# Optimization experiments

Hardware: AMD Instinct MI355X
Metric: run time of the kernel (lower is better)

Reference implementation:

```python
import jax, jax.numpy as jnp
import numpy as np

N_NODES = 100000
N_EDGES = 800000
IN_C, HID_C, OUT_C = 128, 64, 40


def setup_inputs() -> dict:
    key = jax.random.key(0)
    k1, k2, k3, k4, k5, k6 = jax.random.split(key, 6)
    x = jax.random.normal(k1, (N_NODES, IN_C), dtype=jnp.float32)
    edge_index = jax.random.randint(k2, (2, N_EDGES), 0, N_NODES, dtype=jnp.int64)
    W1 = jax.random.normal(k3, (IN_C, HID_C), dtype=jnp.float32) * (1.0 / np.sqrt(IN_C))
    b1 = jax.random.normal(k4, (HID_C,), dtype=jnp.float32) * 0.01
    W2 = jax.random.normal(k5, (HID_C, OUT_C), dtype=jnp.float32) * (1.0 / np.sqrt(HID_C))
    b2 = jax.random.normal(k6, (OUT_C,), dtype=jnp.float32) * 0.01
    return {"x": x, "edge_index": edge_index, "W1": W1, "b1": b1, "W2": W2, "b2": b2}


def _sg_propagate(x, src, dst, n):
    # GCN symmetric normalization (self-loops already appended by caller):
    # deg[i] = number of incoming edges at i; norm_e = deg[src]^-1/2 * deg[dst]^-1/2
    deg = jax.ops.segment_sum(jnp.ones_like(dst, dtype=x.dtype), dst, num_segments=n)
    dinv = jnp.where(deg > 0, jax.lax.rsqrt(deg), jnp.zeros_like(deg))
    norm = dinv[src] * dinv[dst]  # [E]
    # out[i] = sum_{e: dst_e=i} norm_e * x[src_e]
    return jax.ops.segment_sum(x[src] * norm[:, None], dst, num_segments=n)


def reference(x, edge_index, W1, b1, W2, b2):
    n = x.shape[0]
    loop = jnp.arange(n, dtype=edge_index.dtype)
    src = jnp.concatenate([edge_index[0], loop])
    dst = jnp.concatenate([edge_index[1], loop])
    # dropout is identity in eval mode
    h = _sg_propagate(x, src, dst, n) @ W1 + b1   # SGConv(in_c, hid_c), K=1
    h = jax.nn.relu(h)
    o = _sg_propagate(h, src, dst, n) @ W2 + b2   # SGConv(hid_c, out_c), K=1
    return jax.nn.log_softmax(o, axis=1)
```

## Files before the change

kernel.cpp:

```cpp
#include <hip/hip_runtime.h>
#include <math.h>

#define IN_C 128
#define HID_C 64
#define OUT_C 40

typedef unsigned short u16;
__device__ __forceinline__ float bf2f(u16 u) {
  return __uint_as_float(((unsigned int)u) << 16);
}
__device__ __forceinline__ u16 f2bf(float f) {
  unsigned int u = __float_as_uint(f);
  u += 0x7fffu + ((u >> 16) & 1u);
  return (u16)(u >> 16);
}

__global__ void zero4_kernel(int4* __restrict__ p, long long n4) {
  long long i = (long long)blockIdx.x * blockDim.x + threadIdx.x;
  long long stride = (long long)gridDim.x * blockDim.x;
  for (; i < n4; i += stride) p[i] = make_int4(0, 0, 0, 0);
}

__global__ __launch_bounds__(256) void scan1_kernel(
    const int* __restrict__ deg, int* __restrict__ S, int* __restrict__ BS,
    int n) {
  __shared__ int sums[256];
  int t = threadIdx.x;
  int i0 = blockIdx.x * 1024 + t * 4;
  int v0 = (i0 + 0 < n) ? deg[i0 + 0] : 0;
  int v1 = (i0 + 1 < n) ? deg[i0 + 1] : 0;
  int v2 = (i0 + 2 < n) ? deg[i0 + 2] : 0;
  int v3 = (i0 + 3 < n) ? deg[i0 + 3] : 0;
  v1 += v0; v2 += v1; v3 += v2;
  sums[t] = v3;
  __syncthreads();
  for (int off = 1; off < 256; off <<= 1) {
    int x = (t >= off) ? sums[t - off] : 0;
    __syncthreads();
    sums[t] += x;
    __syncthreads();
  }
  int excl = t ? sums[t - 1] : 0;
  if (i0 + 0 < n) S[i0 + 0] = v0 + excl;
  if (i0 + 1 < n) S[i0 + 1] = v1 + excl;
  if (i0 + 2 < n) S[i0 + 2] = v2 + excl;
  if (i0 + 3 < n) S[i0 + 3] = v3 + excl;
  if (t == 255) BS[blockIdx.x] = sums[255];
}

__global__ __launch_bounds__(128) void scan2_kernel(int* __restrict__ BS,
                                                    int nb) {
  __shared__ int s[128];
  int t = threadIdx.x;
  s[t] = (t < nb) ? BS[t] : 0;
  __syncthreads();
  for (int off = 1; off < 128; off <<= 1) {
    int x = (t >= off) ? s[t - off] : 0;
    __syncthreads();
    s[t] += x;
    __syncthreads();
  }
  if (t < nb) BS[t] = t ? s[t - 1] : 0;
}

__global__ void scan3_kernel(const int* __restrict__ S,
                             const int* __restrict__ BS,
                             const int* __restrict__ deg,
                             int* __restrict__ rowptr,
                             float* __restrict__ dinv, int n) {
  int i = blockIdx.x * blockDim.x + threadIdx.x;
  if (i < n) {
    int d = deg[i];
    int r = S[i] + BS[i >> 10];
    rowptr[i + 1] = r;
    dinv[i] = rsqrtf((float)d + 1.0f);
    if (i == 0) rowptr[0] = 0;
  }
}

#define XS_LD 68
#define DP_BLOCKS 1024
__global__ __launch_bounds__(256) void fused_degpos_gemm1_kernel(
    const int* __restrict__ dst, int E, int* __restrict__ deg,
    int* __restrict__ pos, const float* __restrict__ x,
    const float* __restrict__ W1, float* __restrict__ y, int n) {
  __shared__ float xs[64 * XS_LD];
  __shared__ float wsh[64 * HID_C];
  int t = threadIdx.x;
  int b = (int)blockIdx.x;
  bool isDP;
  int bi;
  if (b < 2 * DP_BLOCKS) { isDP = (b & 1) == 0; bi = b >> 1; }
  else                   { isDP = false;        bi = b - DP_BLOCKS; }
  if (isDP) {
    int base = bi * 256 + t;
    int stride = DP_BLOCKS * 256;
    for (int e = base; e < E; e += 4 * stride) {
      int e1 = e + stride, e2 = e + 2 * stride, e3 = e + 3 * stride;
      bool g1 = e1 < E, g2 = e2 < E, g3 = e3 < E;
      int d0 = dst[e];
      int d1 = g1 ? dst[e1] : 0;
      int d2 = g2 ? dst[e2] : 0;
      int d3 = g3 ? dst[e3] : 0;
      int p0 = atomicAdd(&deg[d0], 1);
      int p1 = g1 ? atomicAdd(&deg[d1], 1) : 0;
      int p2 = g2 ? atomicAdd(&deg[d2], 1) : 0;
      int p3 = g3 ? atomicAdd(&deg[d3], 1) : 0;
      pos[e] = p0;
      if (g1) pos[e1] = p1;
      if (g2) pos[e2] = p2;
      if (g3) pos[e3] = p3;
    }
    return;
  }
  int rowBase = bi * 64;
  if (rowBase >= n) return;
  const float4* xf4 = (const float4*)x;
  const float4* wf4 = (const float4*)W1;
  int tx = t & 15, ty = t >> 4;
  int i0 = ty * 4, j0 = tx * 4;
  float acc[4][4];
#pragma unroll
  for (int r = 0; r < 4; ++r)
#pragma unroll
    for (int j = 0; j < 4; ++j) acc[r][j] = 0.f;

  for (int kc = 0; kc < 2; ++kc) {
#pragma unroll
    for (int k = 0; k < 4; ++k) {
      int t4 = t + k * 256;
      int row = t4 >> 4, c4 = t4 & 15;
      int gr = rowBase + row;
      if (gr >= n) gr = n - 1;
      *(float4*)&xs[row * XS_LD + c4 * 4] = xf4[(size_t)gr * 32 + kc * 16 + c4];
      *(float4*)&wsh[row * HID_C + c4 * 4] = wf4[(size_t)(kc * 64 + row) * 16 + c4];
    }
    __syncthreads();
#pragma unroll 2
    for (int c4 = 0; c4 < 64; c4 += 4) {
      float4 xv[4], wv[4];
#pragma unroll
      for (int r = 0; r < 4; ++r)
        xv[r] = *(const float4*)&xs[(i0 + r) * XS_LD + c4];
#pragma unroll
      for (int cc = 0; cc < 4; ++cc)
        wv[cc] = *(const float4*)&wsh[(c4 + cc) * HID_C + j0];
#pragma unroll
      for (int r = 0; r < 4; ++r) {
#pragma unroll
        for (int cc = 0; cc < 4; ++cc) {
          float xr = (&xv[r].x)[cc];
          acc[r][0] = fmaf(xr, wv[cc].x, acc[r][0]);
          acc[r][1] = fmaf(xr, wv[cc].y, acc[r][1]);
          acc[r][2] = fmaf(xr, wv[cc].z, acc[r][2]);
          acc[r][3] = fmaf(xr, wv[cc].w, acc[r][3]);
        }
      }
    }
    __syncthreads();
  }
#pragma unroll
  for (int r = 0; r < 4; ++r) {
    int i = rowBase + i0 + r;
    if (i < n) {
      float4 v = make_float4(acc[r][0], acc[r][1], acc[r][2], acc[r][3]);
      *(float4*)&y[(size_t)i * HID_C + j0] = v;
    }
  }
}

#define FB_BLOCKS 1024
#define SC_BLOCKS 1024
__global__ __launch_bounds__(256) void fused_fill_scale_kernel(
    const int* __restrict__ eidx, int E, const int* __restrict__ rowptr,
    const int* __restrict__ pos, int* __restrict__ csr,
    const float* __restrict__ dinv, const float4* __restrict__ y4,
    ushort4* __restrict__ ybf, int n) {
  int t = threadIdx.x;
  if ((int)blockIdx.x < FB_BLOCKS) {
    int base = blockIdx.x * 256 + t;
    int stride = FB_BLOCKS * 256;
    for (int e = base; e < E; e += 4 * stride) {
      int e1 = e + stride, e2 = e + 2 * stride, e3 = e + 3 * stride;
      bool g1 = e1 < E, g2 = e2 < E, g3 = e3 < E;
      int s0 = eidx[e], d0 = eidx[E + e], p0 = pos[e];
      int s1 = 0, d1 = 0, p1 = 0, s2 = 0, d2 = 0, p2 = 0, s3 = 0, d3 = 0, p3 = 0;
      if (g1) { s1 = eidx[e1]; d1 = eidx[E + e1]; p1 = pos[e1]; }
      if (g2) { s2 = eidx[e2]; d2 = eidx[E + e2]; p2 = pos[e2]; }
      if (g3) { s3 = eidx[e3]; d3 = eidx[E + e3]; p3 = pos[e3]; }
      int r0 = rowptr[d0];
      int r1 = g1 ? rowptr[d1] : 0;
      int r2 = g2 ? rowptr[d2] : 0;
      int r3 = g3 ? rowptr[d3] : 0;
      csr[r0 + p0] = s0;
      if (g1) csr[r1 + p1] = s1;
      if (g2) csr[r2 + p2] = s2;
      if (g3) csr[r3 + p3] = s3;
    }
    return;
  }
  long long total = (long long)n * 16;
  long long base = (long long)((int)blockIdx.x - FB_BLOCKS) * 256 + t;
  long long stride = (long long)SC_BLOCKS * 256;
  for (long long idx = base; idx < total; idx += stride) {
    int i = (int)(idx >> 4);
    float di = dinv[i];
    float4 v = y4[idx];
    ushort4 u;
    u.x = f2bf(di * v.x);
    u.y = f2bf(di * v.y);
    u.z = f2bf(di * v.z);
    u.w = f2bf(di * v.w);
    ybf[idx] = u;
  }
}

__global__ __launch_bounds__(256) void gather1_kernel(
    const ushort4* __restrict__ y4, const int* __restrict__ rowptr,
    const int* __restrict__ csr, const float* __restrict__ dinv,
    const float* __restrict__ b1, float* __restrict__ h, int n) {
  int lane = threadIdx.x & 63;
  int grp = lane >> 4;
  int q = lane & 15;
  float4 b1v = ((const float4*)b1)[q];
  int wid = (int)((blockIdx.x * blockDim.x + threadIdx.x) >> 6);
  int nw = (int)((gridDim.x * blockDim.x) >> 6);
  int ii = wid;
  int e0 = 0, e1 = 0; float di = 0.f;
  if (ii < n) { e0 = rowptr[ii]; e1 = rowptr[ii + 1]; di = dinv[ii]; }
  while (ii < n) {
    int nxt = ii + nw;
    int ne0 = 0, ne1 = 0; float ndi = 0.f;
    if (nxt < n) { ne0 = rowptr[nxt]; ne1 = rowptr[nxt + 1]; ndi = dinv[nxt]; }
    int i = __builtin_amdgcn_readfirstlane(ii);
    float4 acc = make_float4(0.f, 0.f, 0.f, 0.f);
    if (grp == 0) {
      ushort4 u = y4[(size_t)i * 16 + q];
      acc.x = bf2f(u.x); acc.y = bf2f(u.y); acc.z = bf2f(u.z); acc.w = bf2f(u.w);
    }
    int e = e0 + grp, end = e1;
    for (; e + 4 < end; e += 8) {
      int s0 = csr[e], s1 = csr[e + 4];
      ushort4 u0 = y4[(size_t)s0 * 16 + q];
      ushort4 u1 = y4[(size_t)s1 * 16 + q];
      acc.x += bf2f(u0.x) + bf2f(u1.x);
      acc.y += bf2f(u0.y) + bf2f(u1.y);
      acc.z += bf2f(u0.z) + bf2f(u1.z);
      acc.w += bf2f(u0.w) + bf2f(u1.w);
    }
    for (; e < end; e += 4) {
      int s = csr[e];
      ushort4 u = y4[(size_t)s * 16 + q];
      acc.x += bf2f(u.x); acc.y += bf2f(u.y);
      acc.z += bf2f(u.z); acc.w += bf2f(u.w);
    }
    acc.x += __shfl_xor(acc.x, 16); acc.y += __shfl_xor(acc.y, 16);
    acc.z += __shfl_xor(acc.z, 16); acc.w += __shfl_xor(acc.w, 16);
    acc.x += __shfl_xor(acc.x, 32); acc.y += __shfl_xor(acc.y, 32);
    acc.z += __shfl_xor(acc.z, 32); acc.w += __shfl_xor(acc.w, 32);
    if (grp == 0) {
      float4 hv;
      hv.x = fmaxf(fmaf(di, acc.x, b1v.x), 0.f);
      hv.y = fmaxf(fmaf(di, acc.y, b1v.y), 0.f);
      hv.z = fmaxf(fmaf(di, acc.z, b1v.z), 0.f);
      hv.w = fmaxf(fmaf(di, acc.w, b1v.w), 0.f);
      *(float4*)&h[(size_t)i * HID_C + 4 * q] = hv;
    }
    ii = nxt; e0 = ne0; e1 = ne1; di = ndi;
  }
}

__global__ __launch_bounds__(256) void gemm2_kernel(
    const float* __restrict__ h, const float* __restrict__ W2,
    const float* __restrict__ dinv, float* __restrict__ z, int n) {
  __shared__ float hs[64 * XS_LD];
  __shared__ float w2s[64 * OUT_C + 32];
  int t = threadIdx.x;
  int rowBase = blockIdx.x * 64;
  const float4* hf4 = (const float4*)h;
  const float4* wf4 = (const float4*)W2;
#pragma unroll
  for (int k = 0; k < 4; ++k) {
    int t4 = t + k * 256;
    int row = t4 >> 4, c4 = t4 & 15;
    int gr = rowBase + row;
    if (gr >= n) gr = n - 1;
    *(float4*)&hs[row * XS_LD + c4 * 4] = hf4[(size_t)gr * 16 + c4];
  }
  for (int t4 = t; t4 < 640; t4 += 256)
    *(float4*)&w2s[t4 * 4] = wf4[t4];
  __syncthreads();
  int tx = t & 15, ty = t >> 4;
  int i0 = ty * 4, j0 = tx * 4;
  bool active = tx < 10;
  float acc[4][4];
#pragma unroll
  for (int r = 0; r < 4; ++r)
#pragma unroll
    for (int j = 0; j < 4; ++j) acc[r][j] = 0.f;
#pragma unroll 2
  for (int c4 = 0; c4 < 64; c4 += 4) {
    float4 hv[4], wv[4];
#pragma unroll
    for (int r = 0; r < 4; ++r)
      hv[r] = *(const float4*)&hs[(i0 + r) * XS_LD + c4];
#pragma unroll
    for (int cc = 0; cc < 4; ++cc)
      wv[cc] = *(const float4*)&w2s[(c4 + cc) * OUT_C + j0];
#pragma unroll
    for (int r = 0; r < 4; ++r) {
#pragma unroll
      for (int cc = 0; cc < 4; ++cc) {
        float hr = (&hv[r].x)[cc];
        acc[r][0] = fmaf(hr, wv[cc].x, acc[r][0]);
        acc[r][1] = fmaf(hr, wv[cc].y, acc[r][1]);
        acc[r][2] = fmaf(hr, wv[cc].z, acc[r][2]);
        acc[r][3] = fmaf(hr, wv[cc].w, acc[r][3]);
      }
    }
  }
  if (active) {
#pragma unroll
    for (int r = 0; r < 4; ++r) {
      int i = rowBase + i0 + r;
      if (i < n) {
        float d2 = dinv[i];
        float4 v = make_float4(d2 * acc[r][0], d2 * acc[r][1],
                               d2 * acc[r][2], d2 * acc[r][3]);
        *(float4*)&z[(size_t)i * OUT_C + j0] = v;
      }
    }
  }
}

__global__ __launch_bounds__(256) void gather40_kernel(
    const float4* __restrict__ z4, const int* __restrict__ rowptr,
    const int* __restrict__ csr, const float* __restrict__ dinv,
    const float* __restrict__ b2, float* __restrict__ out, int n) {
  int lane = threadIdx.x & 63;
  int grp = lane >> 4;
  int q = lane & 15;
  bool act = q < 10;
  float4 b2v = ((const float4*)b2)[act ? q : 0];
  int wid = (int)((blockIdx.x * blockDim.x + threadIdx.x) >> 6);
  int nw = (int)((gridDim.x * blockDim.x) >> 6);
  int ii = wid;
  int e0 = 0, e1 = 0; float di = 0.f;
  if (ii < n) { e0 = rowptr[ii]; e1 = rowptr[ii + 1]; di = dinv[ii]; }
  while (ii < n) {
    int nxt = ii + nw;
    int ne0 = 0, ne1 = 0; float ndi = 0.f;
    if (nxt < n) { ne0 = rowptr[nxt]; ne1 = rowptr[nxt + 1]; ndi = dinv[nxt]; }
    int i = __builtin_amdgcn_readfirstlane(ii);
    float4 acc = make_float4(0.f, 0.f, 0.f, 0.f);
    if (grp == 0 && act) acc = z4[(size_t)i * 10 + q];
    int e = e0 + grp, end = e1;
    if (act) {
      for (; e + 4 < end; e += 8) {
        int s0 = csr[e], s1 = csr[e + 4];
        float4 v0 = z4[(size_t)s0 * 10 + q];
        float4 v1 = z4[(size_t)s1 * 10 + q];
        acc.x += v0.x + v1.x;
        acc.y += v0.y + v1.y;
        acc.z += v0.z + v1.z;
        acc.w += v0.w + v1.w;
      }
      for (; e < end; e += 4) {
        int s = csr[e];
        float4 v = z4[(size_t)s * 10 + q];
        acc.x += v.x; acc.y += v.y; acc.z += v.z; acc.w += v.w;
      }
    }
    acc.x += __shfl_xor(acc.x, 16); acc.y += __shfl_xor(acc.y, 16);
    acc.z += __shfl_xor(acc.z, 16); acc.w += __shfl_xor(acc.w, 16);
    acc.x += __shfl_xor(acc.x, 32); acc.y += __shfl_xor(acc.y, 32);
    acc.z += __shfl_xor(acc.z, 32); acc.w += __shfl_xor(acc.w, 32);
    float4 o;
    o.x = fmaf(di, acc.x, b2v.x);
    o.y = fmaf(di, acc.y, b2v.y);
    o.z = fmaf(di, acc.z, b2v.z);
    o.w = fmaf(di, acc.w, b2v.w);
    float m = act ? fmaxf(fmaxf(o.x, o.y), fmaxf(o.z, o.w)) : -INFINITY;
    for (int off = 8; off; off >>= 1) m = fmaxf(m, __shfl_xor(m, off));
    float ex = act ? (expf(o.x - m) + expf(o.y - m) +
                      expf(o.z - m) + expf(o.w - m)) : 0.f;
    float s = ex;
    for (int off = 8; off; off >>= 1) s += __shfl_xor(s, off);
    if (lane < 16 && act) {
      float l = m + logf(s);
      float4 o2 = make_float4(o.x - l, o.y - l, o.z - l, o.w - l);
      *(float4*)&out[(size_t)i * OUT_C + 4 * q] = o2;
    }
    ii = nxt; e0 = ne0; e1 = ne1; di = ndi;
  }
}

extern "C" void kernel_launch(void* const* d_in, const int* in_sizes, int n_in,
                              void* d_out, int out_size, void* d_ws, size_t ws_size,
                              hipStream_t stream) {
  const float* x  = (const float*)d_in[0];
  const int* eidx = (const int*)d_in[1];
  const float* W1 = (const float*)d_in[2];
  const float* b1 = (const float*)d_in[3];
  const float* W2 = (const float*)d_in[4];
  const float* b2 = (const float*)d_in[5];
  float* out = (float*)d_out;

  int n = in_sizes[0] / IN_C;
  int E = in_sizes[1] / 2;

  size_t npad = ((size_t)n + 255) & ~(size_t)255;
  size_t Epad = ((size_t)E + 255) & ~(size_t)255;
  size_t o_dinv   = 0;
  size_t o_deg    = o_dinv + npad;
  size_t o_S      = o_deg + npad;
  size_t o_BS     = o_S + npad;
  size_t o_rowptr = o_BS + 256;
  size_t o_pos    = o_rowptr + npad + 256;
  size_t o_csr    = o_pos + Epad;
  size_t o_bufA   = o_csr + Epad;
  size_t o_bufC   = o_bufA + (size_t)n * HID_C;
  size_t needed   = (o_bufC + (size_t)n * HID_C) * 4;
  if (ws_size < needed) return;

  float* ws  = (float*)d_ws;
  float* dinv = ws + o_dinv;
  int* deg    = (int*)(ws + o_deg);
  int* S      = (int*)(ws + o_S);
  int* BS     = (int*)(ws + o_BS);
  int* rowptr = (int*)(ws + o_rowptr);
  int* pos    = (int*)(ws + o_pos);
  int* csr    = (int*)(ws + o_csr);
  float* bufA = ws + o_bufA;
  float* bufC = ws + o_bufC;

  int nb = (int)((n + 1023) / 1024);
  int gemmBlocks = (n + 63) / 64;

  zero4_kernel<<<128, 256, 0, stream>>>((int4*)deg, (long long)(npad / 4));
  fused_degpos_gemm1_kernel<<<DP_BLOCKS + gemmBlocks, 256, 0, stream>>>(
      eidx + E, E, deg, pos, x, W1, bufA, n);

  scan1_kernel<<<nb, 256, 0, stream>>>(deg, S, BS, n);
  scan2_kernel<<<1, 128, 0, stream>>>(BS, nb);
  scan3_kernel<<<(n + 255) / 256, 256, 0, stream>>>(S, BS, deg, rowptr, dinv, n);

  fused_fill_scale_kernel<<<FB_BLOCKS + SC_BLOCKS, 256, 0, stream>>>(
      eidx, E, rowptr, pos, csr, dinv, (const float4*)bufA, (ushort4*)bufC, n);

  gather1_kernel<<<2048, 256, 0, stream>>>((const ushort4*)bufC, rowptr, csr,
                                           dinv, b1, bufA, n);
  gemm2_kernel<<<gemmBlocks, 256, 0, stream>>>(bufA, W2, dinv, bufC, n);
  gather40_kernel<<<2048, 256, 0, stream>>>((const float4*)bufC, rowptr, csr,
                                            dinv, b2, out, n);
}
```

Measured before the change: 166.0 us.

## Store second-layer features as bf16 and gather with 16-byte loads per lane

```diff
diff --git a/kernel.cpp b/kernel.cpp
--- a/kernel.cpp
+++ b/kernel.cpp
@@ -6,13 +6,20 @@
 #define OUT_C 40
 
 typedef unsigned short u16;
-__device__ __forceinline__ float bf2f(u16 u) {
-  return __uint_as_float(((unsigned int)u) << 16);
-}
 __device__ __forceinline__ u16 f2bf(float f) {
   unsigned int u = __float_as_uint(f);
   u += 0x7fffu + ((u >> 16) & 1u);
   return (u16)(u >> 16);
+}
+__device__ __forceinline__ void bf8_add(uint4 u, float* a) {
+  a[0] += __uint_as_float(u.x << 16);
+  a[1] += __uint_as_float(u.x & 0xffff0000u);
+  a[2] += __uint_as_float(u.y << 16);
+  a[3] += __uint_as_float(u.y & 0xffff0000u);
+  a[4] += __uint_as_float(u.z << 16);
+  a[5] += __uint_as_float(u.z & 0xffff0000u);
+  a[6] += __uint_as_float(u.w << 16);
+  a[7] += __uint_as_float(u.w & 0xffff0000u);
 }
 
 __global__ void zero4_kernel(int4* __restrict__ p, long long n4) {
@@ -216,13 +223,14 @@
 }
 
 __global__ __launch_bounds__(256) void gather1_kernel(
-    const ushort4* __restrict__ y4, const int* __restrict__ rowptr,
+    const uint4* __restrict__ y8, const int* __restrict__ rowptr,
     const int* __restrict__ csr, const float* __restrict__ dinv,
     const float* __restrict__ b1, float* __restrict__ h, int n) {
   int lane = threadIdx.x & 63;
-  int grp = lane >> 4;
-  int q = lane & 15;
-  float4 b1v = ((const float4*)b1)[q];
+  int grp = lane >> 3;
+  int q = lane & 7;
+  float4 b1lo = ((const float4*)b1)[2 * q];
+  float4 b1hi = ((const float4*)b1)[2 * q + 1];
   int wid = (int)((blockIdx.x * blockDim.x + threadIdx.x) >> 6);
   int nw = (int)((gridDim.x * blockDim.x) >> 6);
   int ii = wid;
@@ -233,38 +241,36 @@
     int ne0 = 0, ne1 = 0; float ndi = 0.f;
     if (nxt < n) { ne0 = rowptr[nxt]; ne1 = rowptr[nxt + 1]; ndi = dinv[nxt]; }
     int i = __builtin_amdgcn_readfirstlane(ii);
-    float4 acc = make_float4(0.f, 0.f, 0.f, 0.f);
+    float a[8] = {0.f, 0.f, 0.f, 0.f, 0.f, 0.f, 0.f, 0.f};
+    if (grp == 0) bf8_add(y8[(size_t)i * 8 + q], a);
+    int e = e0 + grp, end = e1;
+    for (; e + 8 < end; e += 16) {
+      int s0 = csr[e], s1 = csr[e + 8];
+      bf8_add(y8[(size_t)s0 * 8 + q], a);
+      bf8_add(y8[(size_t)s1 * 8 + q], a);
+    }
+    for (; e < end; e += 8) {
+      int s = csr[e];
+      bf8_add(y8[(size_t)s * 8 + q], a);
+    }
+#pragma unroll
+    for (int k = 0; k < 8; ++k) {
+      a[k] += __shfl_xor(a[k], 8);
+      a[k] += __shfl_xor(a[k], 16);
+      a[k] += __shfl_xor(a[k], 32);
+    }
     if (grp == 0) {
-      ushort4 u = y4[(size_t)i * 16 + q];
-      acc.x = bf2f(u.x); acc.y = bf2f(u.y); acc.z = bf2f(u.z); acc.w = bf2f(u.w);
-    }
-    int e = e0 + grp, end = e1;
-    for (; e + 4 < end; e += 8) {
-      int s0 = csr[e], s1 = csr[e + 4];
-      ushort4 u0 = y4[(size_t)s0 * 16 + q];
-      ushort4 u1 = y4[(size_t)s1 * 16 + q];
-      acc.x += bf2f(u0.x) + bf2f(u1.x);
-      acc.y += bf2f(u0.y) + bf2f(u1.y);
-      acc.z += bf2f(u0.z) + bf2f(u1.z);
-      acc.w += bf2f(u0.w) + bf2f(u1.w);
-    }
-    for (; e < end; e += 4) {
-      int s = csr[e];
-      ushort4 u = y4[(size_t)s * 16 + q];
-      acc.x += bf2f(u.x); acc.y += bf2f(u.y);
-      acc.z += bf2f(u.z); acc.w += bf2f(u.w);
-    }
-    acc.x += __shfl_xor(acc.x, 16); acc.y += __shfl_xor(acc.y, 16);
-    acc.z += __shfl_xor(acc.z, 16); acc.w += __shfl_xor(acc.w, 16);
-    acc.x += __shfl_xor(acc.x, 32); acc.y += __shfl_xor(acc.y, 32);
-    acc.z += __shfl_xor(acc.z, 32); acc.w += __shfl_xor(acc.w, 32);
-    if (grp == 0) {
-      float4 hv;
-      hv.x = fmaxf(fmaf(di, acc.x, b1v.x), 0.f);
-      hv.y = fmaxf(fmaf(di, acc.y, b1v.y), 0.f);
-      hv.z = fmaxf(fmaf(di, acc.z, b1v.z), 0.f);
-      hv.w = fmaxf(fmaf(di, acc.w, b1v.w), 0.f);
-      *(float4*)&h[(size_t)i * HID_C + 4 * q] = hv;
+      float4 lo, hi;
+      lo.x = fmaxf(fmaf(di, a[0], b1lo.x), 0.f);
+      lo.y = fmaxf(fmaf(di, a[1], b1lo.y), 0.f);
+      lo.z = fmaxf(fmaf(di, a[2], b1lo.z), 0.f);
+      lo.w = fmaxf(fmaf(di, a[3], b1lo.w), 0.f);
+      hi.x = fmaxf(fmaf(di, a[4], b1hi.x), 0.f);
+      hi.y = fmaxf(fmaf(di, a[5], b1hi.y), 0.f);
+      hi.z = fmaxf(fmaf(di, a[6], b1hi.z), 0.f);
+      hi.w = fmaxf(fmaf(di, a[7], b1hi.w), 0.f);
+      *(float4*)&h[(size_t)i * HID_C + 8 * q] = lo;
+      *(float4*)&h[(size_t)i * HID_C + 8 * q + 4] = hi;
     }
     ii = nxt; e0 = ne0; e1 = ne1; di = ndi;
   }
@@ -272,7 +278,7 @@
 
 __global__ __launch_bounds__(256) void gemm2_kernel(
     const float* __restrict__ h, const float* __restrict__ W2,
-    const float* __restrict__ dinv, float* __restrict__ z, int n) {
+    const float* __restrict__ dinv, u16* __restrict__ z, int n) {
   __shared__ float hs[64 * XS_LD];
   __shared__ float w2s[64 * OUT_C + 32];
   int t = threadIdx.x;
@@ -325,23 +331,28 @@
       int i = rowBase + i0 + r;
       if (i < n) {
         float d2 = dinv[i];
-        float4 v = make_float4(d2 * acc[r][0], d2 * acc[r][1],
-                               d2 * acc[r][2], d2 * acc[r][3]);
-        *(float4*)&z[(size_t)i * OUT_C + j0] = v;
+        ushort4 u;
+        u.x = f2bf(d2 * acc[r][0]);
+        u.y = f2bf(d2 * acc[r][1]);
+        u.z = f2bf(d2 * acc[r][2]);
+        u.w = f2bf(d2 * acc[r][3]);
+        *(ushort4*)&z[(size_t)i * OUT_C + j0] = u;
       }
     }
   }
 }
 
 __global__ __launch_bounds__(256) void gather40_kernel(
-    const float4* __restrict__ z4, const int* __restrict__ rowptr,
+    const uint4* __restrict__ z8, const int* __restrict__ rowptr,
     const int* __restrict__ csr, const float* __restrict__ dinv,
     const float* __restrict__ b2, float* __restrict__ out, int n) {
   int lane = threadIdx.x & 63;
-  int grp = lane >> 4;
-  int q = lane & 15;
-  bool act = q < 10;
-  float4 b2v = ((const float4*)b2)[act ? q : 0];
+  int grp = lane >> 3;
+  int q = lane & 7;
+  bool act = q < 5;
+  int qc = act ? q : 0;
+  float4 b2lo = ((const float4*)b2)[2 * qc];
+  float4 b2hi = ((const float4*)b2)[2 * qc + 1];
   int wid = (int)((blockIdx.x * blockDim.x + threadIdx.x) >> 6);
   int nw = (int)((gridDim.x * blockDim.x) >> 6);
   int ii = wid;
@@ -352,44 +363,55 @@
     int ne0 = 0, ne1 = 0; float ndi = 0.f;
     if (nxt < n) { ne0 = rowptr[nxt]; ne1 = rowptr[nxt + 1]; ndi = dinv[nxt]; }
     int i = __builtin_amdgcn_readfirstlane(ii);
-    float4 acc = make_float4(0.f, 0.f, 0.f, 0.f);
-    if (grp == 0 && act) acc = z4[(size_t)i * 10 + q];
+    float a[8] = {0.f, 0.f, 0.f, 0.f, 0.f, 0.f, 0.f, 0.f};
+    if (grp == 0 && act) bf8_add(z8[(size_t)i * 5 + q], a);
     int e = e0 + grp, end = e1;
     if (act) {
-      for (; e + 4 < end; e += 8) {
-        int s0 = csr[e], s1 = csr[e + 4];
-        float4 v0 = z4[(size_t)s0 * 10 + q];
-        float4 v1 = z4[(size_t)s1 * 10 + q];
-        acc.x += v0.x + v1.x;
-        acc.y += v0.y + v1.y;
-        acc.z += v0.z + v1.z;
-        acc.w += v0.w + v1.w;
+      for (; e + 8 < end; e += 16) {
+        int s0 = csr[e], s1 = csr[e + 8];
+        bf8_add(z8[(size_t)s0 * 5 + q], a);
+        bf8_add(z8[(size_t)s1 * 5 + q], a);
       }
-      for (; e < end; e += 4) {
+      for (; e < end; e += 8) {
         int s = csr[e];
-        float4 v = z4[(size_t)s * 10 + q];
-        acc.x += v.x; acc.y += v.y; acc.z += v.z; acc.w += v.w;
+        bf8_add(z8[(size_t)s * 5 + q], a);
       }
     }
-    acc.x += __shfl_xor(acc.x, 16); acc.y += __shfl_xor(acc.y, 16);
-    acc.z += __shfl_xor(acc.z, 16); acc.w += __shfl_xor(acc.w, 16);
-    acc.x += __shfl_xor(acc.x, 32); acc.y += __shfl_xor(acc.y, 32);
-    acc.z += __shfl_xor(acc.z, 32); acc.w += __shfl_xor(acc.w, 32);
-    float4 o;
-    o.x = fmaf(di, acc.x, b2v.x);
-    o.y = fmaf(di, acc.y, b2v.y);
-    o.z = fmaf(di, acc.z, b2v.z);
-    o.w = fmaf(di, acc.w, b2v.w);
-    float m = act ? fmaxf(fmaxf(o.x, o.y), fmaxf(o.z, o.w)) : -INFINITY;
-    for (int off = 8; off; off >>= 1) m = fmaxf(m, __shfl_xor(m, off));
-    float ex = act ? (expf(o.x - m) + expf(o.y - m) +
-                      expf(o.z - m) + expf(o.w - m)) : 0.f;
-    float s = ex;
-    for (int off = 8; off; off >>= 1) s += __shfl_xor(s, off);
-    if (lane < 16 && act) {
+#pragma unroll
+    for (int k = 0; k < 8; ++k) {
+      a[k] += __shfl_xor(a[k], 8);
+      a[k] += __shfl_xor(a[k], 16);
+      a[k] += __shfl_xor(a[k], 32);
+    }
+    float o[8];
+    o[0] = fmaf(di, a[0], b2lo.x);
+    o[1] = fmaf(di, a[1], b2lo.y);
+    o[2] = fmaf(di, a[2], b2lo.z);
+    o[3] = fmaf(di, a[3], b2lo.w);
+    o[4] = fmaf(di, a[4], b2hi.x);
+    o[5] = fmaf(di, a[5], b2hi.y);
+    o[6] = fmaf(di, a[6], b2hi.z);
+    o[7] = fmaf(di, a[7], b2hi.w);
+    float m = act ? fmaxf(fmaxf(fmaxf(o[0], o[1]), fmaxf(o[2], o[3])),
+                          fmaxf(fmaxf(o[4], o[5]), fmaxf(o[6], o[7])))
+                  : -INFINITY;
+    m = fmaxf(m, __shfl_xor(m, 1));
+    m = fmaxf(m, __shfl_xor(m, 2));
+    m = fmaxf(m, __shfl_xor(m, 4));
+    float s = 0.f;
+    if (act) {
+#pragma unroll
+      for (int k = 0; k < 8; ++k) s += expf(o[k] - m);
+    }
+    s += __shfl_xor(s, 1);
+    s += __shfl_xor(s, 2);
+    s += __shfl_xor(s, 4);
+    if (lane < 8 && act) {
       float l = m + logf(s);
-      float4 o2 = make_float4(o.x - l, o.y - l, o.z - l, o.w - l);
-      *(float4*)&out[(size_t)i * OUT_C + 4 * q] = o2;
+      float4 lo = make_float4(o[0] - l, o[1] - l, o[2] - l, o[3] - l);
+      float4 hi = make_float4(o[4] - l, o[5] - l, o[6] - l, o[7] - l);
+      *(float4*)&out[(size_t)i * OUT_C + 8 * q] = lo;
+      *(float4*)&out[(size_t)i * OUT_C + 8 * q + 4] = hi;
     }
     ii = nxt; e0 = ne0; e1 = ne1; di = ndi;
   }
@@ -448,9 +470,9 @@
   fused_fill_scale_kernel<<<FB_BLOCKS + SC_BLOCKS, 256, 0, stream>>>(
       eidx, E, rowptr, pos, csr, dinv, (const float4*)bufA, (ushort4*)bufC, n);
 
-  gather1_kernel<<<2048, 256, 0, stream>>>((const ushort4*)bufC, rowptr, csr,
+  gather1_kernel<<<2048, 256, 0, stream>>>((const uint4*)bufC, rowptr, csr,
                                            dinv, b1, bufA, n);
-  gemm2_kernel<<<gemmBlocks, 256, 0, stream>>>(bufA, W2, dinv, bufC, n);
-  gather40_kernel<<<2048, 256, 0, stream>>>((const float4*)bufC, rowptr, csr,
+  gemm2_kernel<<<gemmBlocks, 256, 0, stream>>>(bufA, W2, dinv, (u16*)bufC, n);
+  gather40_kernel<<<2048, 256, 0, stream>>>((const uint4*)bufC, rowptr, csr,
                                             dinv, b2, out, n);
 }
```

Result: slower. 182.2 us (+9.8%).
